# Kernel optimization log

Hardware: AMD Instinct MI355X
Metric: run time of the kernel (lower is better)

## Reference

```python
import jax, jax.numpy as jnp
import numpy as np

SIGMA2_MU = 0.5  # hyper_params['sigma2_mu']
R = 128          # number of spatial basis functions
NV = 2000        # number of query points
KM1 = 30         # K - 1


def setup_inputs() -> dict:
    key = jax.random.key(0)
    k1, k2, k3, k4 = jax.random.split(key, 4)
    Xi_evals = jax.random.normal(k1, (R, NV), dtype=jnp.float32)
    vec_W_post_mean = jax.random.normal(k2, (R * KM1, 1), dtype=jnp.float32)
    vec_W_post_cov = jax.random.normal(k3, (R * KM1, R * KM1), dtype=jnp.float32)
    C_mu = jax.random.normal(k4, (NV, 1), dtype=jnp.float32)
    return {"Xi_evals": Xi_evals, "vec_W_post_mean": vec_W_post_mean,
            "vec_W_post_cov": vec_W_post_cov, "C_mu": C_mu}


def reference(Xi_evals, vec_W_post_mean, vec_W_post_cov, C_mu):
    # Xi_evals: (r, Nv); vec_W_post_mean: (r*(K-1), 1); vec_W_post_cov: (r*(K-1), r*(K-1))
    r, Nv = Xi_evals.shape
    Km1 = vec_W_post_mean.shape[0] // r
    K = Km1 + 1
    X = Xi_evals.T                                # (Nv, r)
    # kron(x^T, I_{K-1}) @ w  ==  X @ W  with W = w.reshape(r, K-1)
    W = vec_W_post_mean.reshape(r, Km1)
    Post_mean_c = X @ W                           # (Nv, K-1)
    # kron(x^T, I) @ Cov @ kron(x, I): quadratic form over r-blocks
    C4 = vec_W_post_cov.reshape(r, Km1, r, Km1)   # (i, k, j, l)
    A = jnp.einsum('vi,ikjl->vkjl', X, C4)        # (Nv, K-1, r, K-1)
    Post_cov_c = jnp.einsum('vkjl,vj->vkl', A, X) # (Nv, K-1, K-1)
    Post_mean_coefs = jnp.concatenate([C_mu, Post_mean_c], axis=1)  # (Nv, K)
    Post_cov_mats = jnp.zeros((Nv, K, K), dtype=Xi_evals.dtype)
    Post_cov_mats = Post_cov_mats.at[:, 0, 0].set(SIGMA2_MU)
    Post_cov_mats = Post_cov_mats.at[:, 1:, 1:].set(Post_cov_c)
    return Post_mean_coefs, Post_cov_mats
```

## Files before the change

kernel.cpp:

```cpp
#include <hip/hip_runtime.h>

typedef _Float16 f16;
typedef _Float16 f16x8 __attribute__((ext_vector_type(8)));
typedef float    f32x16 __attribute__((ext_vector_type(16)));

#define NV      2000
#define RR      128
#define KM1     30
#define KKOUT   31
#define NQ      900
#define QQ      961
#define COV_OFF 62000

#define B5_BYTES 17104896
#define XH_BYTES 524288

#define PERM_BLKS  3840
#define XC1_BLKS   128
#define ZERO_BLKS  1877
#define MEAN_BLKS  248
#define PREP_GRID  (PERM_BLKS + XC1_BLKS + ZERO_BLKS + MEAN_BLKS)

__global__ void prep_kernel(const float* __restrict__ Xi,
                            const float* __restrict__ Wm,
                            const float* __restrict__ cov,
                            const float* __restrict__ Cmu,
                            f16* __restrict__ B5,
                            f16* __restrict__ Xh,
                            float* __restrict__ outm,
                            float* __restrict__ oc) {
    __shared__ float rowS[3840];
    int b = blockIdx.x, tid = threadIdx.x;
    if (b < PERM_BLKS) {
        int i = b / 30, k = b - i * 30;
        int g = i >> 4;
        int j0 = g << 4;
        int W = 128 - j0;
        int lo = (i - j0) * 30;
        const float* src = cov + (size_t)b * 3840 + j0 * 30;
        for (int t = tid; t < W * 30; t += 256)
            rowS[t] = (t >= lo) ? src[t] : 0.f;
        __syncthreads();
        int n2 = (127 - i) * 15;
        for (int idx = tid; idx < n2; idx += 256) {
            int j = i + 1 + idx / 15;
            int p = idx - (j - i - 1) * 15;
            const float2 v2 = *(const float2*)(cov + (size_t)(j * 30 + k) * 3840 + i * 30 + 2 * p);
            rowS[(j - j0) * 30 + 2 * p]     += v2.x;
            rowS[(j - j0) * 30 + 2 * p + 1] += v2.y;
        }
        __syncthreads();
        int t_st = i & 15;
        int nOct = W >> 3;
        for (int it = tid; it < nOct * 30; it += 256) {
            int oct = it / 30, l = it - oct * 30;
            int j = j0 + oct * 8;
            int s = j >> 4, kq = (j >> 3) & 1;
            int q = k * 30 + l, qt = q >> 5, l31 = q & 31;
            int kz, slot;
            if (g < 4) { kz = g;     slot = s - g; }
            else       { kz = 7 - g; slot = s + 1; }
            f16 vals[8];
#pragma unroll
            for (int d = 0; d < 8; ++d) vals[d] = (f16)rowS[(j + d - j0) * 30 + l];
            f16* dst = B5 + ((((size_t)(qt * 4 + kz) * 16 + t_st) * 9 + slot) << 9)
                          + (kq * 32 + l31) * 8;
            *(uint4*)dst = *(uint4*)vals;
        }
        return;
    }
    b -= PERM_BLKS;
    if (b < XC1_BLKS) {
        int t = b * 256 + tid;
        int v = t & 2047, rc = t >> 11;
        f16 vals[8];
#pragma unroll
        for (int d = 0; d < 8; ++d) {
            float x = (v < NV) ? Xi[(rc * 8 + d) * NV + v] : 0.f;
            vals[d] = (f16)x;
        }
        *(uint4*)(Xh + (size_t)v * 128 + rc * 8) = *(uint4*)vals;
        return;
    }
    b -= XC1_BLKS;
    if (b < ZERO_BLKS) {
        size_t idx = ((size_t)b * 256 + tid) * 4;
        if (idx < (size_t)NV * QQ) {
            unsigned rem = (unsigned)(idx % QQ);
            float4 zv;
            zv.x = (rem == 0u)   ? 0.5f : 0.f;
            zv.y = (rem == 960u) ? 0.5f : 0.f;
            zv.z = (rem == 959u) ? 0.5f : 0.f;
            zv.w = (rem == 958u) ? 0.5f : 0.f;
            *(float4*)(oc + idx) = zv;
        }
        return;
    }
    b -= ZERO_BLKS;
    int t2 = b * 256 + tid;
    int c = t2 >> 11, v = t2 & 2047;
    if (v >= NV || c >= KKOUT) return;
    if (c == 0) { outm[(size_t)v * KKOUT] = Cmu[v]; return; }
    float acc = 0.f;
    const float* w = Wm + (c - 1);
#pragma unroll 8
    for (int i = 0; i < RR; ++i)
        acc = fmaf(Xi[i * NV + v], w[i * KM1], acc);
    outm[(size_t)v * KKOUT + c] = acc;
}

template<int KZ>
__device__ __forceinline__ void gemm_body(const f16* __restrict__ B5,
                                          const f16* __restrict__ Xh,
                                          float* __restrict__ out_cov,
                                          int qt, int y) {
    constexpr int NA = 8 - KZ, NB = 1 + KZ, NS = 8 - KZ, UB = 7 - 2 * KZ;
    const int tid = threadIdx.x, lane = tid & 63, w = tid >> 6;
    const int l31 = lane & 31, kq = lane >> 5;
    const int v0 = y * 512 + w * 128;
    const int vr = v0 + l31;

    f16x8 xj[4][NS];
#pragma unroll
    for (int fm = 0; fm < 4; ++fm)
#pragma unroll
        for (int u = 0; u < NS; ++u)
            xj[fm][u] = *(const f16x8*)(Xh + (size_t)(vr + fm * 32) * 128 + (KZ + u) * 16 + kq * 8);

    const f16* gbase = B5 + ((size_t)(qt * 4 + KZ) * 16) * 4608 + lane * 8;

    f32x16 acc[4] = {};

#pragma unroll
    for (int t = 0; t < 16; ++t) {
        f16x8 bfv[9];
#pragma unroll
        for (int m = 0; m < 9; ++m)
            bfv[m] = *(const f16x8*)(gbase + (size_t)t * 4608 + m * 512);

        const int srcl = l31 + ((t >> 3) << 5);
        f16 xA[4], xB[4];
#pragma unroll
        for (int fm = 0; fm < 4; ++fm) {
            unsigned short ha = __builtin_bit_cast(unsigned short, (f16)xj[fm][0][t & 7]);
            unsigned short hb = __builtin_bit_cast(unsigned short, (f16)xj[fm][UB][t & 7]);
            int pa = __shfl((int)ha, srcl, 64);
            int pb = __shfl((int)hb, srcl, 64);
            xA[fm] = __builtin_bit_cast(f16, (unsigned short)pa);
            xB[fm] = __builtin_bit_cast(f16, (unsigned short)pb);
        }
#pragma unroll
        for (int m = 0; m < NA; ++m) {
#pragma unroll
            for (int fm = 0; fm < 4; ++fm)
                acc[fm] = __builtin_amdgcn_mfma_f32_32x32x16_f16(xj[fm][m] * xA[fm], bfv[m], acc[fm], 0, 0, 0);
        }
#pragma unroll
        for (int m2 = 0; m2 < NB; ++m2) {
#pragma unroll
            for (int fm = 0; fm < 4; ++fm)
                acc[fm] = __builtin_amdgcn_mfma_f32_32x32x16_f16(xj[fm][UB + m2] * xB[fm], bfv[NA + m2], acc[fm], 0, 0, 0);
        }
    }

    const int q = qt * 32 + l31;
    if (q >= NQ) return;
    const int kk = q / 30, ll = q - kk * 30;
    float* cb = out_cov + (kk + 1) * KKOUT + (ll + 1);
#pragma unroll
    for (int fm = 0; fm < 4; ++fm) {
        int vb = v0 + fm * 32 + 4 * kq;
#pragma unroll
        for (int r = 0; r < 16; ++r) {
            int v = vb + (r & 3) + 8 * (r >> 2);
            if (v < NV) atomicAdd(cb + (size_t)v * QQ, acc[fm][r]);
        }
    }
}

__launch_bounds__(256, 2)
__global__ void gemm5_kernel(const f16* __restrict__ B5,
                             const f16* __restrict__ Xh,
                             float* __restrict__ out_cov) {
    const int bid = blockIdx.x;
    const int xcd = bid & 7, base = bid >> 3;
    const int y = base & 3, s3 = base >> 2;
    const int S = s3 * 8 + xcd;
    const int qt = S >> 2, kz = S & 3;
    if (qt >= 29) return;
    switch (kz) {
        case 0:  gemm_body<0>(B5, Xh, out_cov, qt, y); break;
        case 1:  gemm_body<1>(B5, Xh, out_cov, qt, y); break;
        case 2:  gemm_body<2>(B5, Xh, out_cov, qt, y); break;
        default: gemm_body<3>(B5, Xh, out_cov, qt, y); break;
    }
}

extern "C" void kernel_launch(void* const* d_in, const int* in_sizes, int n_in,
                              void* d_out, int out_size, void* d_ws, size_t ws_size,
                              hipStream_t stream) {
    const float* Xi  = (const float*)d_in[0];
    const float* Wm  = (const float*)d_in[1];
    const float* Cov = (const float*)d_in[2];
    const float* Cmu = (const float*)d_in[3];
    float* out      = (float*)d_out;
    float* out_mean = out;
    float* out_cov  = out + COV_OFF;
    f16* B5 = (f16*)d_ws;
    f16* Xh = (f16*)((char*)d_ws + B5_BYTES);

    prep_kernel <<<PREP_GRID, 256, 0, stream>>>(Xi, Wm, Cov, Cmu, B5, Xh,
                                                out_mean, out_cov);
    gemm5_kernel<<<480, 256, 0, stream>>>(B5, Xh, out_cov);
}
```

Measured before the change: 176.1 us.

## Merge kz split into one block with double-buffered B loads and plain stores

Each block now runs all four kz sections itself instead of splitting them across blocks. Because no other block contributes to an output element, the float atomicAdds become plain stores. The per-block v tile shrinks from 128 to 64 rows per wave (two accumulators). B fragments are double-buffered so the next stage's loads overlap the current MFMAs. The grid drops from 480 to 232 blocks at one block per CU, which removes atomic traffic but lowers occupancy and parallelism.

```diff
diff --git a/kernel.cpp b/kernel.cpp
--- a/kernel.cpp
+++ b/kernel.cpp
@@ -109,90 +109,98 @@
     outm[(size_t)v * KKOUT + c] = acc;
 }
 
+__device__ __forceinline__ void load9(f16x8 (&b)[9], const f16* p) {
+#pragma unroll
+    for (int m = 0; m < 9; ++m)
+        b[m] = *(const f16x8*)(p + m * 512);
+}
+
 template<int KZ>
-__device__ __forceinline__ void gemm_body(const f16* __restrict__ B5,
-                                          const f16* __restrict__ Xh,
-                                          float* __restrict__ out_cov,
-                                          int qt, int y) {
-    constexpr int NA = 8 - KZ, NB = 1 + KZ, NS = 8 - KZ, UB = 7 - 2 * KZ;
+__device__ __forceinline__ void stage_compute(int t, int l31,
+                                              const f16x8 (&bv)[9],
+                                              const f16x8 (&xj)[2][8],
+                                              f32x16 (&acc)[2]) {
+    constexpr int NA = 8 - KZ, NB = 1 + KZ;
+    const int srcl = l31 + ((t >> 3) << 5);
+    f16 xA[2], xB[2];
+#pragma unroll
+    for (int fm = 0; fm < 2; ++fm) {
+        unsigned short ha = __builtin_bit_cast(unsigned short, (f16)xj[fm][KZ][t & 7]);
+        unsigned short hb = __builtin_bit_cast(unsigned short, (f16)xj[fm][7 - KZ][t & 7]);
+        int pa = __shfl((int)ha, srcl, 64);
+        int pb = __shfl((int)hb, srcl, 64);
+        xA[fm] = __builtin_bit_cast(f16, (unsigned short)pa);
+        xB[fm] = __builtin_bit_cast(f16, (unsigned short)pb);
+    }
+#pragma unroll
+    for (int m = 0; m < NA; ++m)
+#pragma unroll
+        for (int fm = 0; fm < 2; ++fm)
+            acc[fm] = __builtin_amdgcn_mfma_f32_32x32x16_f16(xj[fm][KZ + m] * xA[fm], bv[m], acc[fm], 0, 0, 0);
+#pragma unroll
+    for (int m2 = 0; m2 < NB; ++m2)
+#pragma unroll
+        for (int fm = 0; fm < 2; ++fm)
+            acc[fm] = __builtin_amdgcn_mfma_f32_32x32x16_f16(xj[fm][7 - KZ + m2] * xB[fm], bv[NA + m2], acc[fm], 0, 0, 0);
+}
+
+template<int KZ>
+__device__ __forceinline__ void kz_section(const f16*& gs,
+                                           f16x8 (&cur)[9], f16x8 (&nxt)[9],
+                                           const f16x8 (&xj)[2][8],
+                                           f32x16 (&acc)[2], int l31) {
+#pragma unroll
+    for (int tt = 0; tt < 8; ++tt) {
+        load9(nxt, gs); gs += 4608;
+        stage_compute<KZ>(2 * tt, l31, cur, xj, acc);
+        load9(cur, gs); gs += 4608;
+        stage_compute<KZ>(2 * tt + 1, l31, nxt, xj, acc);
+    }
+}
+
+__launch_bounds__(256, 1)
+__global__ void gemm6_kernel(const f16* __restrict__ B5,
+                             const f16* __restrict__ Xh,
+                             float* __restrict__ out_cov) {
+    const int bid = blockIdx.x;
+    const int p = (bid & 7) * 29 + (bid >> 3);
+    const int qt = p >> 3, y = p & 7;
     const int tid = threadIdx.x, lane = tid & 63, w = tid >> 6;
     const int l31 = lane & 31, kq = lane >> 5;
-    const int v0 = y * 512 + w * 128;
+    const int v0 = y * 256 + w * 64;
     const int vr = v0 + l31;
 
-    f16x8 xj[4][NS];
-#pragma unroll
-    for (int fm = 0; fm < 4; ++fm)
-#pragma unroll
-        for (int u = 0; u < NS; ++u)
-            xj[fm][u] = *(const f16x8*)(Xh + (size_t)(vr + fm * 32) * 128 + (KZ + u) * 16 + kq * 8);
-
-    const f16* gbase = B5 + ((size_t)(qt * 4 + KZ) * 16) * 4608 + lane * 8;
-
-    f32x16 acc[4] = {};
-
-#pragma unroll
-    for (int t = 0; t < 16; ++t) {
-        f16x8 bfv[9];
-#pragma unroll
-        for (int m = 0; m < 9; ++m)
-            bfv[m] = *(const f16x8*)(gbase + (size_t)t * 4608 + m * 512);
-
-        const int srcl = l31 + ((t >> 3) << 5);
-        f16 xA[4], xB[4];
-#pragma unroll
-        for (int fm = 0; fm < 4; ++fm) {
-            unsigned short ha = __builtin_bit_cast(unsigned short, (f16)xj[fm][0][t & 7]);
-            unsigned short hb = __builtin_bit_cast(unsigned short, (f16)xj[fm][UB][t & 7]);
-            int pa = __shfl((int)ha, srcl, 64);
-            int pb = __shfl((int)hb, srcl, 64);
-            xA[fm] = __builtin_bit_cast(f16, (unsigned short)pa);
-            xB[fm] = __builtin_bit_cast(f16, (unsigned short)pb);
-        }
-#pragma unroll
-        for (int m = 0; m < NA; ++m) {
-#pragma unroll
-            for (int fm = 0; fm < 4; ++fm)
-                acc[fm] = __builtin_amdgcn_mfma_f32_32x32x16_f16(xj[fm][m] * xA[fm], bfv[m], acc[fm], 0, 0, 0);
-        }
-#pragma unroll
-        for (int m2 = 0; m2 < NB; ++m2) {
-#pragma unroll
-            for (int fm = 0; fm < 4; ++fm)
-                acc[fm] = __builtin_amdgcn_mfma_f32_32x32x16_f16(xj[fm][UB + m2] * xB[fm], bfv[NA + m2], acc[fm], 0, 0, 0);
-        }
-    }
+    f16x8 xj[2][8];
+#pragma unroll
+    for (int fm = 0; fm < 2; ++fm)
+#pragma unroll
+        for (int u = 0; u < 8; ++u)
+            xj[fm][u] = *(const f16x8*)(Xh + (size_t)(vr + fm * 32) * 128 + u * 16 + kq * 8);
+
+    const f16* gbase = B5 + (size_t)qt * 64 * 4608 + lane * 8;
+
+    f16x8 cur[9], nxt[9];
+    load9(cur, gbase);
+    const f16* gs = gbase + 4608;
+
+    f32x16 acc[2] = {};
+    kz_section<0>(gs, cur, nxt, xj, acc, l31);
+    kz_section<1>(gs, cur, nxt, xj, acc, l31);
+    kz_section<2>(gs, cur, nxt, xj, acc, l31);
+    kz_section<3>(gs, cur, nxt, xj, acc, l31);
 
     const int q = qt * 32 + l31;
     if (q >= NQ) return;
     const int kk = q / 30, ll = q - kk * 30;
     float* cb = out_cov + (kk + 1) * KKOUT + (ll + 1);
 #pragma unroll
-    for (int fm = 0; fm < 4; ++fm) {
+    for (int fm = 0; fm < 2; ++fm) {
         int vb = v0 + fm * 32 + 4 * kq;
 #pragma unroll
         for (int r = 0; r < 16; ++r) {
             int v = vb + (r & 3) + 8 * (r >> 2);
-            if (v < NV) atomicAdd(cb + (size_t)v * QQ, acc[fm][r]);
-        }
-    }
-}
-
-__launch_bounds__(256, 2)
-__global__ void gemm5_kernel(const f16* __restrict__ B5,
-                             const f16* __restrict__ Xh,
-                             float* __restrict__ out_cov) {
-    const int bid = blockIdx.x;
-    const int xcd = bid & 7, base = bid >> 3;
-    const int y = base & 3, s3 = base >> 2;
-    const int S = s3 * 8 + xcd;
-    const int qt = S >> 2, kz = S & 3;
-    if (qt >= 29) return;
-    switch (kz) {
-        case 0:  gemm_body<0>(B5, Xh, out_cov, qt, y); break;
-        case 1:  gemm_body<1>(B5, Xh, out_cov, qt, y); break;
-        case 2:  gemm_body<2>(B5, Xh, out_cov, qt, y); break;
-        default: gemm_body<3>(B5, Xh, out_cov, qt, y); break;
+            if (v < NV) cb[(size_t)v * QQ] = acc[fm][r];
+        }
     }
 }
 
@@ -211,5 +219,5 @@
 
     prep_kernel <<<PREP_GRID, 256, 0, stream>>>(Xi, Wm, Cov, Cmu, B5, Xh,
                                                 out_mean, out_cov);
-    gemm5_kernel<<<480, 256, 0, stream>>>(B5, Xh, out_cov);
-}
+    gemm6_kernel<<<232, 256, 0, stream>>>(B5, Xh, out_cov);
+}
```

Measured after the change: 155.6 us. 11.6% less time.
